# Kernel optimization log

Hardware: AMD Instinct MI355X
Metric: run time of the kernel (lower is better)

The kernel has to match this reference:

```python
import jax, jax.numpy as jnp
import numpy as np

P, N, M, B = 5, 30000, 50000, 256
T, C, L, ED, H, EMB, TD, NL = 13, 16, 3, 4, 128, 64, 5, 3
SRC = jnp.repeat(jnp.arange(P), P)  # edge type i = src*P + dst
DST = jnp.tile(jnp.arange(P), P)


def _affine(x, W, b):
    # x: [P, n, i], W: [P, i, o], b: [P, o]
    return jnp.einsum('pni,pio->pno', x, W) + b[:, None, :]


def _lrelu(x, s=0.01):
    return jnp.where(x >= 0, x, s * x)


def _gat(h, W, a_s, a_d, We, a_e, b, edge_index, edge_attr):
    # h: [P, N, H]; per-edge-type GATConv (heads=1, no self loops) then hetero 'max' aggregation
    hs, hd = h[SRC], h[DST]                       # [25, N, H]
    xl = jnp.einsum('enh,ehf->enf', hs, W)        # transformed source features
    xr = jnp.einsum('enh,ehf->enf', hd, W)
    als = jnp.einsum('enf,ef->en', xl, a_s)
    ald = jnp.einsum('enf,ef->en', xr, a_d)

    def per_type(xl_e, als_e, ald_e, ea, We_e, ae_e, ei):
        src, dst = ei[0], ei[1]
        alpha = als_e[src] + ald_e[dst] + (ea @ We_e) @ ae_e
        alpha = jnp.where(alpha >= 0, alpha, 0.2 * alpha)  # GAT negative_slope=0.2
        amax = jax.ops.segment_max(alpha, dst, num_segments=N)
        ex = jnp.exp(alpha - amax[dst])
        den = jax.ops.segment_sum(ex, dst, num_segments=N)
        w = ex / (den[dst] + 1e-16)
        return jax.ops.segment_sum(w[:, None] * xl_e[src], dst, num_segments=N)

    out = jax.vmap(per_type)(xl, als, ald, edge_attr, We, a_e, edge_index)
    out = out + b[:, None, :]
    return out.reshape(P, P, N, H).max(axis=0)  # HeteroConv aggr='max' over source types


def setup_inputs():
    key = jax.random.key(0)
    ks = iter(jax.random.split(key, 64))
    def nrm(shape, s=1.0):
        return jax.random.normal(next(ks), shape, dtype=jnp.float32) * s
    w = 0.05
    inp = {
        'x': nrm((P, N, T)),
        'cond_x': nrm((P, N, C + L)),
        'edge_attr': nrm((P * P, M, ED)),
        'timesteps': jax.random.uniform(next(ks), (B,), dtype=jnp.float32),
        'te1_W': nrm((1, TD), w), 'te1_b': nrm((TD,), w),
        'te2_W': nrm((TD, TD), w), 'te2_b': nrm((TD,), w),
        'emb_W': nrm((P, T + L, EMB), w), 'emb_b': nrm((P, EMB), w),
        'cemb_W': nrm((P, C, EMB), w), 'cemb_b': nrm((P, EMB), w),
        'pa_W': nrm((P, 2 * EMB, 2 * EMB), w), 'pa_b': nrm((P, 2 * EMB), w),
        'pc_W': nrm((P, 2 * EMB, EMB), w), 'pc_b': nrm((P, EMB), w),
        'sl0_W': nrm((P, EMB + TD, H), w), 'sl0_b': nrm((P, H), w),
        'sl12_W': nrm((2, P, H + TD, H), w), 'sl12_b': nrm((2, P, H), w),
        'slout_W': nrm((P, H + TD, T), w), 'slout_b': nrm((P, T), w),
        'gat_W': nrm((NL, P * P, H, H), w), 'gat_as': nrm((NL, P * P, H), w),
        'gat_ad': nrm((NL, P * P, H), w), 'gat_We': nrm((NL, P * P, ED, H), w),
        'gat_ae': nrm((NL, P * P, H), w), 'gat_b': nrm((NL, P * P, H), w),
        'xc_W': nrm((NL, P, H, H // 2), w), 'xc_b': nrm((NL, P, H // 2), w),
        'cc_W': nrm((NL, P, H, H // 2), w), 'cc_b': nrm((NL, P, H // 2), w),
        'ca_W': nrm((NL, P, H, H), w), 'ca_b': nrm((NL, P, H), w),
        'batch_idx': jax.random.randint(next(ks), (P, N), 0, B),
        'edge_index': jax.random.randint(next(ks), (P * P, 2, M), 0, N),
    }
    return inp


def reference(x, cond_x, edge_attr, timesteps, te1_W, te1_b, te2_W, te2_b,
              emb_W, emb_b, cemb_W, cemb_b, pa_W, pa_b, pc_W, pc_b,
              sl0_W, sl0_b, sl12_W, sl12_b, slout_W, slout_b,
              gat_W, gat_as, gat_ad, gat_We, gat_ae, gat_b,
              xc_W, xc_b, cc_W, cc_b, ca_W, ca_b, batch_idx, edge_index):
    # time embedding: Linear(1,TD) -> SiLU -> Linear(TD,TD)
    temb = jax.nn.silu(timesteps[:, None] @ te1_W + te1_b) @ te2_W + te2_b  # [B, TD]
    cond, latent = cond_x[..., :C], cond_x[..., C:]
    h = _affine(jnp.concatenate([x, latent], -1), emb_W, emb_b)            # [P,N,EMB]
    ce = _affine(cond, cemb_W, cemb_b)
    h = jnp.concatenate([h, ce], -1)                                       # [P,N,2EMB]
    h = jax.nn.sigmoid(_affine(h, pa_W, pa_b)) * h                         # attention pooling
    h = _affine(h, pc_W, pc_b)                                             # [P,N,EMB]
    nt = temb[batch_idx]                                                   # [P,N,TD]
    h = jnp.concatenate([h, nt], -1)
    for l in range(NL):
        if l > 0:
            h = jnp.concatenate([h, nt], -1)
        Wl, bl = (sl0_W, sl0_b) if l == 0 else (sl12_W[l - 1], sl12_b[l - 1])
        h = _lrelu(_affine(h, Wl, bl))                                     # [P,N,H]
        comm = _lrelu(_gat(h, gat_W[l], gat_as[l], gat_ad[l], gat_We[l], gat_ae[l], gat_b[l], edge_index, edge_attr))
        h = jnp.concatenate([_affine(h, xc_W[l], xc_b[l]), _affine(comm, cc_W[l], cc_b[l])], -1)
        h = h + jax.nn.sigmoid(_affine(h, ca_W[l], ca_b[l])) * h
    h = jnp.concatenate([h, nt], -1)
    return _affine(h, slout_W, slout_b)                                    # [P,N,T]
```

## Files before the change

### kernel.cpp

```cpp
#include <hip/hip_runtime.h>
#include <cstdio>

using bf8 = __attribute__((ext_vector_type(8))) short;
using f4v = __attribute__((ext_vector_type(4))) float;
typedef unsigned short u16;
typedef unsigned int u32;

#define DEV __device__ __forceinline__

DEV float bf2f(u16 u){ return __uint_as_float(((u32)u) << 16); }
DEV u16 f2bf(float f){ u32 u = __float_as_uint(f); return (u16)((u + 0x7fffu + ((u >> 16) & 1u)) >> 16); }
DEV float sigm(float v){ return 1.f / (1.f + __expf(-v)); }

constexpr int P5 = 5, NN = 30000, MM = 50000, NE = 25, BB = 256;
constexpr int KC = 96;
constexpr int RS = KC * 2 + 16;
constexpr int RSA = 272;

__global__ void temb_k(const float* ts, const float* w1, const float* b1,
                       const float* w2, const float* b2, float* temb){
  int i = blockIdx.x * blockDim.x + threadIdx.x;
  if (i >= BB) return;
  float t = ts[i]; float z[5];
#pragma unroll
  for (int j = 0; j < 5; ++j){ float u = t * w1[j] + b1[j]; z[j] = u * sigm(u); }
#pragma unroll
  for (int j2 = 0; j2 < 5; ++j2){
    float s = b2[j2];
#pragma unroll
    for (int j = 0; j < 5; ++j) s += z[j] * w2[j * 5 + j2];
    temb[i * 5 + j2] = s;
  }
}

__global__ void wtransE_k(const float* __restrict__ W, u16* __restrict__ Wt,
                          int Kreal, int Kpad, int Nreal, int Nalloc, int total){
  int idx = blockIdx.x * blockDim.x + threadIdx.x;
  if (idx >= total) return;
  int k = idx % Kpad;
  int t2 = idx / Kpad;
  int f = t2 % Nalloc;
  int b = t2 / Nalloc;
  float v = (k < Kreal && f < Nreal) ? W[((size_t)b * Kreal + k) * Nreal + f] : 0.f;
  Wt[idx] = f2bf(v);
}

__global__ void embw_k(const float* emb_W, const float* emb_b, const float* cemb_W, const float* cemb_b,
                       u16* Wc, float* bc){
  int b = blockIdx.x, f = threadIdx.x;
  for (int k = 0; k < 32; ++k){
    float v = 0.f;
    if (f < 64){ if (k < 16) v = emb_W[((size_t)b * 16 + k) * 64 + f]; }
    else       { if (k >= 16) v = cemb_W[((size_t)b * 16 + (k - 16)) * 64 + (f - 64)]; }
    Wc[((size_t)b * 128 + f) * 32 + k] = f2bf(v);
  }
  bc[b * 128 + f] = (f < 64) ? emb_b[b * 64 + f] : cemb_b[b * 64 + (f - 64)];
}

__global__ void gwtT_k(const float* __restrict__ gW, u16* __restrict__ gWt){
  int idx = blockIdx.x * blockDim.x + threadIdx.x;
  if (idx >= 75 * 128 * 128) return;
  int h = idx & 127, f = (idx >> 7) & 127, le = idx >> 14;
  gWt[idx] = f2bf(gW[(size_t)le * 16384 + h * 128 + f]);
}

__global__ void gatred_k(const float* gW, const float* gas, const float* gad,
                         const float* gWe, const float* gae,
                         float* wswd, float* eaw){
  int le = blockIdx.x; int h = threadIdx.x;
  const float* W = gW + (size_t)le * 16384;
  const float* as_ = gas + le * 128;
  const float* ad_ = gad + le * 128;
  float wsv = 0.f, wdv = 0.f;
  for (int f = 0; f < 128; ++f){
    float w = W[h * 128 + f];
    wsv += w * as_[f]; wdv += w * ad_[f];
  }
  wswd[le * 256 + h] = wsv;
  wswd[le * 256 + 128 + h] = wdv;
  if (h < 4){
    const float* We = gWe + (size_t)le * 512;
    const float* ae = gae + le * 128;
    float s = 0.f;
    for (int f = 0; f < 128; ++f) s += We[h * 128 + f] * ae[f];
    eaw[le * 4 + h] = s;
  }
}

__global__ void abuild_k(const float* x, const float* cx, u16* A0){
  int idx = blockIdx.x * blockDim.x + threadIdx.x;
  if (idx >= P5 * NN) return;
  const float* xr = x + (size_t)idx * 13;
  const float* cr = cx + (size_t)idx * 19;
  u16* a0 = A0 + (size_t)idx * 32;
#pragma unroll
  for (int i = 0; i < 13; ++i) a0[i] = f2bf(xr[i]);
#pragma unroll
  for (int i = 0; i < 3; ++i) a0[13 + i] = f2bf(cr[16 + i]);
#pragma unroll
  for (int i = 0; i < 16; ++i) a0[16 + i] = f2bf(cr[i]);
}

__global__ void ntfill_k(u16* buf, int pitch, int co, const int* bidx, const float* temb){
  int idx = blockIdx.x * blockDim.x + threadIdx.x;
  if (idx >= P5 * NN) return;
  int b = bidx[idx];
  u16* r = buf + (size_t)idx * pitch;
#pragma unroll
  for (int j = 0; j < 5; ++j) r[co + j] = f2bf(temb[b * 5 + j]);
  for (int j = co + 5; j < pitch; ++j) r[j] = 0;
}

__global__ void csr_count_k(const int* EI, int* cnt){
  int idx = blockIdx.x * blockDim.x + threadIdx.x;
  if (idx >= NE * MM) return;
  int e = idx / MM, m = idx % MM;
  int dst = EI[(size_t)e * 2 * MM + MM + m];
  atomicAdd(&cnt[e * NN + dst], 1);
}

__global__ __launch_bounds__(1024) void csr_scan_k(const int* cnt, int* off){
  int e = blockIdx.x, tid = threadIdx.x;
  int lane = tid & 63, wv = tid >> 6;
  __shared__ int wsum[16];
  int running = 0;
  for (int c = 0; c < 30; ++c){
    int idx = c * 1024 + tid;
    int v = (idx < NN) ? cnt[e * NN + idx] : 0;
    int s = v;
#pragma unroll
    for (int o = 1; o < 64; o <<= 1){
      int t = __shfl_up(s, o, 64);
      if (lane >= o) s += t;
    }
    if (lane == 63) wsum[wv] = s;
    __syncthreads();
    if (wv == 0 && lane < 16){
      int t = wsum[lane];
#pragma unroll
      for (int o = 1; o < 16; o <<= 1){
        int u = __shfl_up(t, o, 64);
        if (lane >= o) t += u;
      }
      wsum[lane] = t;
    }
    __syncthreads();
    int base = running + ((wv > 0) ? wsum[wv - 1] : 0);
    if (idx < NN) off[(size_t)e * (NN + 1) + idx] = base + s - v;
    running += wsum[15];
    __syncthreads();
  }
  if (tid == 0) off[(size_t)e * (NN + 1) + NN] = running;
}

__global__ void csr_fill_k(const int* EI, const int* off, int* cnt, int* mpos){
  int idx = blockIdx.x * blockDim.x + threadIdx.x;
  if (idx >= NE * MM) return;
  int e = idx / MM, m = idx % MM;
  int dst = EI[(size_t)e * 2 * MM + MM + m];
  int pos = off[(size_t)e * (NN + 1) + dst] + atomicAdd(&cnt[e * NN + dst], 1);
  mpos[idx] = pos;
}

__global__ __launch_bounds__(256) void dots2_k(const u16* __restrict__ hS, const float* __restrict__ wswd_l,
                                               float* __restrict__ als, float* __restrict__ ald){
  __shared__ u32 hl[64][65];
  __shared__ float wsl[10][129];
  int p = blockIdx.y;
  int n0 = blockIdx.x * 64;
  int tid = threadIdx.x;
  for (int i = tid; i < 10 * 128; i += 256){
    int col = i >> 7, k = i & 127;
    int e = (col < 5) ? (p * 5 + col) : ((col - 5) * 5 + p);
    wsl[col][k] = wswd_l[e * 256 + ((col < 5) ? 0 : 128) + k];
  }
  for (int i = tid; i < 64 * 64; i += 256){
    int r = i >> 6, kp = i & 63;
    int n = n0 + r;
    hl[r][kp] = (n < NN) ? ((const u32*)hS)[((size_t)p * NN + n) * 64 + kp] : 0u;
  }
  __syncthreads();
  int col = tid & 15, rbase = tid >> 4;
  if (col < 10){
#pragma unroll
    for (int pass = 0; pass < 4; ++pass){
      int r = rbase + pass * 16;
      int n = n0 + r;
      if (n >= NN) continue;
      float s = 0.f;
#pragma unroll
      for (int kp = 0; kp < 64; ++kp){
        u32 pr = hl[r][kp];
        s += bf2f((u16)(pr & 0xffffu)) * wsl[col][2 * kp]
           + bf2f((u16)(pr >> 16)) * wsl[col][2 * kp + 1];
      }
      if (col < 5) als[(size_t)(p * 5 + col) * NN + n] = s;
      else         ald[(size_t)((col - 5) * 5 + p) * NN + n] = s;
    }
  }
}

__global__ __launch_bounds__(256) void alpha_k(const int* EI, const float* ea, const float* als,
                                               const float* ald, const float* eaw_l,
                                               float* alpha, u32* amax){
  int idx = blockIdx.x * blockDim.x + threadIdx.x;
  if (idx >= NE * MM) return;
  int e = idx / MM, m = idx % MM;
  int src = EI[(size_t)e * 2 * MM + m];
  int dst = EI[(size_t)e * 2 * MM + MM + m];
  const float* a4 = ea + ((size_t)e * MM + m) * 4;
  const float* ew = eaw_l + e * 4;
  float a = als[(size_t)e * NN + src] + ald[(size_t)e * NN + dst]
          + a4[0] * ew[0] + a4[1] * ew[1] + a4[2] * ew[2] + a4[3] * ew[3];
  a = (a >= 0.f) ? a : 0.2f * a;
  alpha[(size_t)e * MM + m] = a;
  u32 ua = __float_as_uint(a);
  u32 enc = (ua & 0x80000000u) ? ~ua : (ua | 0x80000000u);
  atomicMax(&amax[(size_t)e * NN + dst], enc);
}

__global__ __launch_bounds__(256) void exprec_k(const int* EI, const float* alpha, const u32* amax,
                                                const int* mpos, uint2* prec){
  int idx = blockIdx.x * blockDim.x + threadIdx.x;
  if (idx >= NE * MM) return;
  int e = idx / MM, m = idx - e * MM;
  int src = EI[(size_t)e * 2 * MM + m];
  int dst = EI[(size_t)e * 2 * MM + MM + m];
  u32 enc = amax[(size_t)e * NN + dst];
  float am = (enc & 0x80000000u) ? __uint_as_float(enc & 0x7fffffffu) : __uint_as_float(~enc);
  float ex = __expf(alpha[idx] - am);
  uint2 pr; pr.x = (u32)src; pr.y = __float_as_uint(ex);
  prec[(size_t)e * MM + mpos[idx]] = pr;
}

__global__ __launch_bounds__(256) void agg3_k(const u16* __restrict__ hS, const uint2* __restrict__ prec,
                                              const int* __restrict__ off, u16* __restrict__ agghB,
                                              int pd0, int npd){
  int l = threadIdx.x & 63, w = threadIdx.x >> 6;
  int n0 = blockIdx.x * 8 + w;
  int n1 = n0 + 4;
  int y = blockIdx.y;
  int ps = y / npd, e = ps * 5 + pd0 + (y - ps * npd);
  const uint2* pe = prec + (size_t)e * MM;
  const int* offe = off + (size_t)e * (NN + 1);
  const u32* hb = (const u32*)hS + (size_t)ps * NN * 64 + l;
  int ro0 = 0, ln0 = 0, ro1 = 0, ln1 = 0;
  if (n0 < NN){ ro0 = offe[n0]; ln0 = offe[n0 + 1] - ro0; }
  if (n1 < NN){ ro1 = offe[n1]; ln1 = offe[n1 + 1] - ro1; }
  float den0 = 0.f, a00 = 0.f, a01 = 0.f;
  float den1 = 0.f, a10 = 0.f, a11 = 0.f;
  int mx = (ln0 > ln1) ? ln0 : ln1;
  for (int t = 0; t < mx; ++t){
    if (t < ln0){
      uint2 pr = pe[ro0 + t];
      float ex = __uint_as_float(pr.y);
      u32 hv = hb[(size_t)pr.x * 64];
      den0 += ex; a00 += ex * bf2f((u16)(hv & 0xffffu)); a01 += ex * bf2f((u16)(hv >> 16));
    }
    if (t < ln1){
      uint2 pr = pe[ro1 + t];
      float ex = __uint_as_float(pr.y);
      u32 hv = hb[(size_t)pr.x * 64];
      den1 += ex; a10 += ex * bf2f((u16)(hv & 0xffffu)); a11 += ex * bf2f((u16)(hv >> 16));
    }
  }
  if (n0 < NN){
    float inv = 1.f / (den0 + 1e-16f);
    ((u32*)agghB)[((size_t)y * NN + n0) * 64 + l] = (u32)f2bf(a00 * inv) | ((u32)f2bf(a01 * inv) << 16);
  }
  if (n1 < NN){
    float inv = 1.f / (den1 + 1e-16f);
    ((u32*)agghB)[((size_t)y * NN + n1) * 64 + l] = (u32)f2bf(a10 * inv) | ((u32)f2bf(a11 * inv) << 16);
  }
}

template<int NF, int MI, int NJ, int EPI, bool ALRELU>
__global__ __launch_bounds__(256) void tgemm_k(const u16* __restrict__ A, const u16* __restrict__ Wt,
                                               const float* __restrict__ bias, void* __restrict__ out,
                                               const u16* __restrict__ X,
                                               int Kpad, int opitch, int ocol, int xpitch){
  constexpr int Nalloc = NF * 16;
  constexpr int WR = 128 / (MI * 16);
  constexpr int WC = 4 / WR;
  static_assert(WR * WC == 4 && NJ * WC * 16 == Nalloc, "wave tiling");
  extern __shared__ __align__(16) char smem[];
  float* Cs = (float*)smem;
  const int tid = threadIdx.x;
  const int l = tid & 63, w = tid >> 6;
  const int bz = blockIdx.z;
  const int r0 = blockIdx.x * 128;
  const int wr = w / WC, wc = w % WC;
  const size_t Ab = (size_t)bz * NN;

  f4v acc[MI][NJ];
#pragma unroll
  for (int i = 0; i < MI; ++i)
#pragma unroll
    for (int j = 0; j < NJ; ++j) acc[i][j] = f4v{0.f, 0.f, 0.f, 0.f};

  for (int kb = 0; kb < Kpad; kb += KC){
    int kc = Kpad - kb; if (kc > KC) kc = KC;
    int nseg = kc >> 3;
    for (int s = tid; s < 128 * nseg; s += 256){
      int r = s / nseg, c = s - r * nseg;
      int grow = r0 + r; if (grow > NN - 1) grow = NN - 1;
      uint4 v = *(const uint4*)(A + (Ab + grow) * Kpad + kb + c * 8);
      if (ALRELU){
        u32 pr[4] = {v.x, v.y, v.z, v.w};
#pragma unroll
        for (int q = 0; q < 4; ++q){
          float lo = bf2f((u16)(pr[q] & 0xffffu)), hi = bf2f((u16)(pr[q] >> 16));
          lo = lo >= 0.f ? lo : 0.01f * lo; hi = hi >= 0.f ? hi : 0.01f * hi;
          pr[q] = (u32)f2bf(lo) | ((u32)f2bf(hi) << 16);
        }
        v.x = pr[0]; v.y = pr[1]; v.z = pr[2]; v.w = pr[3];
      }
      *(uint4*)(smem + r * RS + c * 16) = v;
    }
    for (int s = tid; s < Nalloc * nseg; s += 256){
      int r = s / nseg, c = s - r * nseg;
      uint4 v = *(const uint4*)(Wt + ((size_t)bz * Nalloc + r) * Kpad + kb + c * 8);
      *(uint4*)(smem + 128 * RS + r * RS + c * 16) = v;
    }
    __syncthreads();
    int KI = kc >> 5;
    for (int k0 = 0; k0 < KI; ++k0){
      bf8 af[MI], bfr[NJ];
#pragma unroll
      for (int i = 0; i < MI; ++i){
        int row = wr * (MI * 16) + i * 16 + (l & 15);
        af[i] = *(const bf8*)(smem + row * RS + k0 * 64 + (l >> 4) * 16);
      }
#pragma unroll
      for (int j = 0; j < NJ; ++j){
        int col = wc * (NJ * 16) + j * 16 + (l & 15);
        bfr[j] = *(const bf8*)(smem + 128 * RS + col * RS + k0 * 64 + (l >> 4) * 16);
      }
#pragma unroll
      for (int i = 0; i < MI; ++i)
#pragma unroll
        for (int j = 0; j < NJ; ++j)
          acc[i][j] = __builtin_amdgcn_mfma_f32_16x16x32_bf16(af[i], bfr[j], acc[i][j], 0, 0, 0);
    }
    __syncthreads();
  }

  if (EPI == 4){
    int col = l & 15;
    if (col < 13){
#pragma unroll
      for (int i = 0; i < MI; ++i){
        float bv = bias[bz * 13 + col];
#pragma unroll
        for (int r = 0; r < 4; ++r){
          int grow = r0 + wr * (MI * 16) + i * 16 + (l >> 4) * 4 + r;
          if (grow < NN)
            ((float*)out)[((size_t)bz * NN + grow) * 13 + col] = acc[i][0][r] + bv;
        }
      }
    }
    return;
  }

#pragma unroll
  for (int i = 0; i < MI; ++i)
#pragma unroll
    for (int j = 0; j < NJ; ++j){
      int tcol = wc * (NJ * 16) + j * 16 + (l & 15);
      float bv = bias[bz * Nalloc + tcol];
#pragma unroll
      for (int r = 0; r < 4; ++r){
        int trow = wr * (MI * 16) + i * 16 + (l >> 4) * 4 + r;
        float v = acc[i][j][r] + bv;
        if (EPI == 2) v = v >= 0.f ? v : 0.01f * v;
        Cs[trow * Nalloc + tcol] = v;
      }
    }
  __syncthreads();
  constexpr int nsc = Nalloc / 4;
  u16* o16 = (u16*)out;
  for (int s = tid; s < 128 * nsc; s += 256){
    int r = s / nsc, c = s - r * nsc;
    int grow = r0 + r; if (grow >= NN) continue;
    float4 cv = *(const float4*)(Cs + r * Nalloc + c * 4);
    float v0 = cv.x, v1 = cv.y, v2 = cv.z, v3 = cv.w;
    if (EPI == 1 || EPI == 3){
      uint2 xv = *(const uint2*)(X + ((size_t)bz * NN + grow) * xpitch + c * 4);
      float x0 = bf2f((u16)(xv.x & 0xffffu)), x1 = bf2f((u16)(xv.x >> 16));
      float x2 = bf2f((u16)(xv.y & 0xffffu)), x3 = bf2f((u16)(xv.y >> 16));
      if (EPI == 1){ v0 = x0 * sigm(v0); v1 = x1 * sigm(v1); v2 = x2 * sigm(v2); v3 = x3 * sigm(v3); }
      else { v0 = x0 * (1.f + sigm(v0)); v1 = x1 * (1.f + sigm(v1)); v2 = x2 * (1.f + sigm(v2)); v3 = x3 * (1.f + sigm(v3)); }
    }
    uint2 ov;
    ov.x = (u32)f2bf(v0) | ((u32)f2bf(v1) << 16);
    ov.y = (u32)f2bf(v2) | ((u32)f2bf(v3) << 16);
    *(uint2*)(o16 + ((size_t)bz * NN + grow) * opitch + ocol + c * 4) = ov;
  }
}

__global__ __launch_bounds__(256) void tgatmm_k(const u16* __restrict__ agghB, const u16* __restrict__ gWt_l,
                                                const float* __restrict__ gb_l, u16* __restrict__ comm,
                                                int pd){
  extern __shared__ __align__(16) char smem[];
  char* As = smem;
  char* Bs = smem + 128 * RSA;
  float* Cs = (float*)smem;
  const int tid = threadIdx.x, l = tid & 63, w = tid >> 6;
  const int r0 = blockIdx.x * 128;
  const int wr = w >> 1, wc = w & 1;
  f4v vmax[4][4];
#pragma unroll 1
  for (int ps = 0; ps < 5; ++ps){
    int e = ps * 5 + pd;
    const u16* aggs = agghB + (size_t)ps * NN * 128;
    const u16* wb = gWt_l + (size_t)e * 16384;
    for (int s = tid; s < 128 * 16; s += 256){
      int r = s >> 4, c = s & 15;
      int grow = r0 + r; if (grow > NN - 1) grow = NN - 1;
      *(uint4*)(As + r * RSA + c * 16) = *(const uint4*)(aggs + (size_t)grow * 128 + c * 8);
      *(uint4*)(Bs + r * RSA + c * 16) = *(const uint4*)(wb + r * 128 + c * 8);
    }
    __syncthreads();
    f4v acc[4][4];
#pragma unroll
    for (int i = 0; i < 4; ++i)
#pragma unroll
      for (int j = 0; j < 4; ++j) acc[i][j] = f4v{0.f, 0.f, 0.f, 0.f};
#pragma unroll
    for (int k0 = 0; k0 < 4; ++k0){
      bf8 af[4], bfr[4];
#pragma unroll
      for (int i = 0; i < 4; ++i)
        af[i] = *(const bf8*)(As + (wr * 64 + i * 16 + (l & 15)) * RSA + k0 * 64 + (l >> 4) * 16);
#pragma unroll
      for (int j = 0; j < 4; ++j)
        bfr[j] = *(const bf8*)(Bs + (wc * 64 + j * 16 + (l & 15)) * RSA + k0 * 64 + (l >> 4) * 16);
#pragma unroll
      for (int i = 0; i < 4; ++i)
#pragma unroll
        for (int j = 0; j < 4; ++j)
          acc[i][j] = __builtin_amdgcn_mfma_f32_16x16x32_bf16(af[i], bfr[j], acc[i][j], 0, 0, 0);
    }
    const float* be = gb_l + e * 128;
#pragma unroll
    for (int i = 0; i < 4; ++i)
#pragma unroll
      for (int j = 0; j < 4; ++j){
        int tcol = wc * 64 + j * 16 + (l & 15);
        float bv = be[tcol];
#pragma unroll
        for (int r = 0; r < 4; ++r){
          float cvv = acc[i][j][r] + bv;
          vmax[i][j][r] = (ps == 0) ? cvv : fmaxf(vmax[i][j][r], cvv);
        }
      }
    __syncthreads();
  }
#pragma unroll
  for (int i = 0; i < 4; ++i)
#pragma unroll
    for (int j = 0; j < 4; ++j){
      int tcol = wc * 64 + j * 16 + (l & 15);
#pragma unroll
      for (int r = 0; r < 4; ++r){
        int trow = wr * 64 + i * 16 + (l >> 4) * 4 + r;
        Cs[trow * 128 + tcol] = vmax[i][j][r];
      }
    }
  __syncthreads();
  for (int s = tid; s < 128 * 32; s += 256){
    int r = s >> 5, c = s & 31;
    int grow = r0 + r; if (grow >= NN) continue;
    float4 cv = *(const float4*)(Cs + r * 128 + c * 4);
    uint2 ov;
    ov.x = (u32)f2bf(cv.x) | ((u32)f2bf(cv.y) << 16);
    ov.y = (u32)f2bf(cv.z) | ((u32)f2bf(cv.w) << 16);
    *(uint2*)(comm + ((size_t)pd * NN + grow) * 128 + c * 4) = ov;
  }
}

constexpr size_t ALN(size_t x){ return (x + 255) & ~(size_t)255; }
constexpr size_t SZ_A0   = ALN((size_t)P5 * NN * 32 * 2);
constexpr size_t SZ_H0   = ALN((size_t)P5 * NN * 96 * 2);
constexpr size_t SZ_H128 = ALN((size_t)P5 * NN * 128 * 2);
constexpr size_t SZ_HL   = ALN((size_t)P5 * NN * 160 * 2);
constexpr size_t O_A0 = 0;
constexpr size_t O_H0 = O_A0 + SZ_A0;
constexpr size_t O_AGG = 0;
constexpr size_t O_HCAT = O_H0 + SZ_H0;
constexpr size_t O_HG = O_HCAT + SZ_H128;
constexpr size_t O_HS = O_HG + SZ_H128;
constexpr size_t O_HL = O_HS + SZ_H128;
constexpr size_t O_TEMB = O_HL + SZ_HL;
constexpr size_t O_WSWD = O_TEMB + ALN(256 * 5 * 4);
constexpr size_t O_EAW  = O_WSWD + ALN(75 * 256 * 4);
constexpr size_t O_CNT  = O_EAW + ALN(75 * 4 * 4);
constexpr size_t O_OFFS = O_CNT + ALN((size_t)NE * NN * 4);
constexpr size_t O_MPOS = O_OFFS + ALN((size_t)NE * (NN + 1) * 4);
constexpr size_t O_ALS  = O_MPOS + ALN((size_t)NE * MM * 4);
constexpr size_t O_ALD  = O_ALS + ALN((size_t)NE * NN * 4);
constexpr size_t O_ALPHA= O_ALD + ALN((size_t)NE * NN * 4);
constexpr size_t O_AMAX = O_ALPHA + ALN((size_t)NE * MM * 4);
constexpr size_t O_GWT  = O_AMAX + ALN((size_t)NE * NN * 4);
constexpr size_t O_WCMB = O_GWT + ALN((size_t)75 * 16384 * 2);
constexpr size_t O_BCMB = O_WCMB + ALN((size_t)5 * 128 * 32 * 2);
constexpr size_t O_WPA  = O_BCMB + ALN((size_t)5 * 128 * 4);
constexpr size_t O_WPC  = O_WPA + ALN((size_t)5 * 128 * 128 * 2);
constexpr size_t O_WSL0 = O_WPC + ALN((size_t)5 * 64 * 128 * 2);
constexpr size_t O_WSL12= O_WSL0 + ALN((size_t)5 * 128 * 96 * 2);
constexpr size_t O_WSLO = O_WSL12 + ALN((size_t)10 * 128 * 160 * 2);
constexpr size_t O_WXC  = O_WSLO + ALN((size_t)5 * 16 * 160 * 2);
constexpr size_t O_WCC  = O_WXC + ALN((size_t)15 * 64 * 128 * 2);
constexpr size_t O_WCA  = O_WCC + ALN((size_t)15 * 64 * 128 * 2);
constexpr size_t O_PREC = O_WCA + ALN((size_t)15 * 128 * 128 * 2);
constexpr size_t WS_NEED= O_PREC + ALN((size_t)NE * MM * 8);

extern "C" void kernel_launch(void* const* d_in, const int* in_sizes, int n_in,
                              void* d_out, int out_size, void* d_ws, size_t ws_size,
                              hipStream_t stream){
  if (ws_size < WS_NEED){
    fprintf(stderr, "kernel_launch: ws too small: need %zu have %zu\n", WS_NEED, ws_size);
    return;
  }
  const float* x        = (const float*)d_in[0];
  const float* cond_x   = (const float*)d_in[1];
  const float* edge_attr= (const float*)d_in[2];
  const float* timesteps= (const float*)d_in[3];
  const float* te1_W = (const float*)d_in[4];
  const float* te1_b = (const float*)d_in[5];
  const float* te2_W = (const float*)d_in[6];
  const float* te2_b = (const float*)d_in[7];
  const float* emb_W = (const float*)d_in[8];
  const float* emb_b = (const float*)d_in[9];
  const float* cemb_W= (const float*)d_in[10];
  const float* cemb_b= (const float*)d_in[11];
  const float* pa_W  = (const float*)d_in[12];
  const float* pa_b  = (const float*)d_in[13];
  const float* pc_W  = (const float*)d_in[14];
  const float* pc_b  = (const float*)d_in[15];
  const float* sl0_W = (const float*)d_in[16];
  const float* sl0_b = (const float*)d_in[17];
  const float* sl12_W= (const float*)d_in[18];
  const float* sl12_b= (const float*)d_in[19];
  const float* slout_W=(const float*)d_in[20];
  const float* slout_b=(const float*)d_in[21];
  const float* gat_W = (const float*)d_in[22];
  const float* gat_as= (const float*)d_in[23];
  const float* gat_ad= (const float*)d_in[24];
  const float* gat_We= (const float*)d_in[25];
  const float* gat_ae= (const float*)d_in[26];
  const float* gat_b = (const float*)d_in[27];
  const float* xc_W  = (const float*)d_in[28];
  const float* xc_b  = (const float*)d_in[29];
  const float* cc_W  = (const float*)d_in[30];
  const float* cc_b  = (const float*)d_in[31];
  const float* ca_W  = (const float*)d_in[32];
  const float* ca_b  = (const float*)d_in[33];
  const int* batch_idx = (const int*)d_in[34];
  const int* edge_index= (const int*)d_in[35];

  char* ws = (char*)d_ws;
  u16* A0    = (u16*)(ws + O_A0);
  u16* h0buf = (u16*)(ws + O_H0);
  u16* agghB = (u16*)(ws + O_AGG);
  u16* hcat  = (u16*)(ws + O_HCAT);
  u16* hg    = (u16*)(ws + O_HG);
  u16* h2    = (u16*)(ws + O_HG);
  u16* hS    = (u16*)(ws + O_HS);
  u16* hL    = (u16*)(ws + O_HL);
  u16* comm  = (u16*)(ws + O_HL);
  float* tembp = (float*)(ws + O_TEMB);
  float* wswdp = (float*)(ws + O_WSWD);
  float* eawp  = (float*)(ws + O_EAW);
  int* cnt  = (int*)(ws + O_CNT);
  int* offs = (int*)(ws + O_OFFS);
  int* mposp= (int*)(ws + O_MPOS);
  float* alsp = (float*)(ws + O_ALS);
  float* aldp = (float*)(ws + O_ALD);
  float* alphap = (float*)(ws + O_ALPHA);
  u32* amaxp = (u32*)(ws + O_AMAX);
  u16* gwt   = (u16*)(ws + O_GWT);
  u16* wcmb  = (u16*)(ws + O_WCMB);
  float* bcmb= (float*)(ws + O_BCMB);
  u16* wpa   = (u16*)(ws + O_WPA);
  u16* wpc   = (u16*)(ws + O_WPC);
  u16* wsl0  = (u16*)(ws + O_WSL0);
  u16* wsl12 = (u16*)(ws + O_WSL12);
  u16* wslo  = (u16*)(ws + O_WSLO);
  u16* wxc   = (u16*)(ws + O_WXC);
  u16* wcc   = (u16*)(ws + O_WCC);
  u16* wca   = (u16*)(ws + O_WCA);
  uint2* precp = (uint2*)(ws + O_PREC);

  const dim3 B256(256);
  const dim3 TG(235, 1, 5);
  const int GPN = (P5 * NN + 255) / 256;
  const int GEM = (NE * MM + 255) / 256;
  constexpr int LDS_N128 = 65536;
  constexpr int LDS_N64  = 39936;
  constexpr int LDS_SLO  = 29952;
  constexpr int LDS_TGAT = 128 * RSA * 2;

  temb_k<<<1, B256, 0, stream>>>(timesteps, te1_W, te1_b, te2_W, te2_b, tembp);
  embw_k<<<5, 128, 0, stream>>>(emb_W, emb_b, cemb_W, cemb_b, wcmb, bcmb);
  {
    auto WT = [&](const float* W, u16* Wt, int Kr, int Kp, int Nr, int Na, int B){
      int total = B * Na * Kp;
      wtransE_k<<<(total + 255) / 256, B256, 0, stream>>>(W, Wt, Kr, Kp, Nr, Na, total);
    };
    WT(pa_W, wpa, 128, 128, 128, 128, 5);
    WT(pc_W, wpc, 128, 128, 64, 64, 5);
    WT(sl0_W, wsl0, 69, 96, 128, 128, 5);
    WT(sl12_W, wsl12, 133, 160, 128, 128, 10);
    WT(slout_W, wslo, 133, 160, 13, 16, 5);
    WT(xc_W, wxc, 128, 128, 64, 64, 15);
    WT(cc_W, wcc, 128, 128, 64, 64, 15);
    WT(ca_W, wca, 128, 128, 128, 128, 15);
  }
  gwtT_k<<<(75 * 128 * 128 + 255) / 256, B256, 0, stream>>>(gat_W, gwt);
  gatred_k<<<75, 128, 0, stream>>>(gat_W, gat_as, gat_ad, gat_We, gat_ae, wswdp, eawp);

  hipMemsetAsync(cnt, 0, (size_t)NE * NN * 4, stream);
  csr_count_k<<<GEM, B256, 0, stream>>>(edge_index, cnt);
  csr_scan_k<<<25, 1024, 0, stream>>>(cnt, offs);
  hipMemsetAsync(cnt, 0, (size_t)NE * NN * 4, stream);
  csr_fill_k<<<GEM, B256, 0, stream>>>(edge_index, offs, cnt, mposp);

  abuild_k<<<GPN, B256, 0, stream>>>(x, cond_x, A0);
  tgemm_k<8, 4, 4, 0, false><<<TG, B256, LDS_N128, stream>>>(A0, wcmb, bcmb, hcat, nullptr, 32, 128, 0, 0);
  tgemm_k<8, 4, 4, 1, false><<<TG, B256, LDS_N128, stream>>>(hcat, wpa, pa_b, hg, hcat, 128, 128, 0, 128);
  tgemm_k<4, 2, 4, 0, false><<<TG, B256, LDS_N64, stream>>>(hg, wpc, pc_b, h0buf, nullptr, 128, 96, 0, 0);
  ntfill_k<<<GPN, B256, 0, stream>>>(h0buf, 96, 64, batch_idx, tembp);

  for (int l = 0; l < 3; ++l){
    if (l == 0)
      tgemm_k<8, 4, 4, 2, false><<<TG, B256, LDS_N128, stream>>>(h0buf, wsl0, sl0_b, hS, nullptr, 96, 128, 0, 0);
    else
      tgemm_k<8, 4, 4, 2, false><<<TG, B256, LDS_N128, stream>>>(hL, wsl12 + (size_t)(l - 1) * 5 * 128 * 160,
                                                                 sl12_b + (size_t)(l - 1) * 5 * 128, hS, nullptr,
                                                                 160, 128, 0, 0);
    const float* wswd_l = wswdp + (size_t)l * 25 * 256;
    const float* eaw_l = eawp + (size_t)l * 25 * 4;
    const u16* gwt_l = gwt + (size_t)l * 25 * 16384;
    const float* gb_l = gat_b + (size_t)l * 25 * 128;
    dots2_k<<<dim3(469, 5), B256, 0, stream>>>(hS, wswd_l, alsp, aldp);
    hipMemsetAsync(amaxp, 0, (size_t)NE * NN * 4, stream);
    alpha_k<<<GEM, B256, 0, stream>>>(edge_index, edge_attr, alsp, aldp, eaw_l, alphap, amaxp);
    exprec_k<<<GEM, B256, 0, stream>>>(edge_index, alphap, amaxp, mposp, precp);
    for (int pd = 0; pd < 5; ++pd){
      agg3_k<<<dim3(3750, 5), B256, 0, stream>>>(hS, precp, offs, agghB, pd, 1);
      tgatmm_k<<<dim3(235), B256, LDS_TGAT, stream>>>(agghB, gwt_l, gb_l, comm, pd);
    }
    tgemm_k<4, 2, 4, 0, false><<<TG, B256, LDS_N64, stream>>>(hS, wxc + (size_t)l * 5 * 64 * 128,
                                                              xc_b + (size_t)l * 5 * 64, h2, nullptr,
                                                              128, 128, 0, 0);
    tgemm_k<4, 2, 4, 0, true><<<TG, B256, LDS_N64, stream>>>(comm, wcc + (size_t)l * 5 * 64 * 128,
                                                             cc_b + (size_t)l * 5 * 64, h2, nullptr,
                                                             128, 128, 64, 0);
    tgemm_k<8, 4, 4, 3, false><<<TG, B256, LDS_N128, stream>>>(h2, wca + (size_t)l * 5 * 128 * 128,
                                                               ca_b + (size_t)l * 5 * 128, hL, h2,
                                                               128, 160, 0, 128);
    ntfill_k<<<GPN, B256, 0, stream>>>(hL, 160, 128, batch_idx, tembp);
  }

  tgemm_k<1, 2, 1, 4, false><<<TG, B256, LDS_SLO, stream>>>(hL, wslo, slout_b, d_out, nullptr, 160, 13, 0, 0);
}
```

Measured before the change: 2.061 ms.

## Compute GAT softmax per destination via CSR, removing atomics and alpha buffer

```diff
diff --git a/kernel.cpp b/kernel.cpp
--- a/kernel.cpp
+++ b/kernel.cpp
@@ -153,13 +153,27 @@
   if (tid == 0) off[(size_t)e * (NN + 1) + NN] = running;
 }
 
-__global__ void csr_fill_k(const int* EI, const int* off, int* cnt, int* mpos){
+__global__ void csr_fill_k(const int* EI, const int* off, int* cnt, int* mpos, int* srcC){
   int idx = blockIdx.x * blockDim.x + threadIdx.x;
   if (idx >= NE * MM) return;
   int e = idx / MM, m = idx % MM;
   int dst = EI[(size_t)e * 2 * MM + MM + m];
   int pos = off[(size_t)e * (NN + 1) + dst] + atomicAdd(&cnt[e * NN + dst], 1);
   mpos[idx] = pos;
+  srcC[(size_t)e * MM + pos] = EI[(size_t)e * 2 * MM + m];
+}
+
+__global__ void eadot_k(const float* __restrict__ ea, const float* __restrict__ eaw,
+                        const int* __restrict__ mpos, float* __restrict__ eadot){
+  int idx = blockIdx.x * blockDim.x + threadIdx.x;
+  if (idx >= 3 * NE * MM) return;
+  int l = idx / (NE * MM);
+  int rem = idx - l * NE * MM;
+  int e = rem / MM, m = rem - e * MM;
+  const float* a4 = ea + ((size_t)e * MM + m) * 4;
+  const float* ew = eaw + (size_t)(l * NE + e) * 4;
+  float d = a4[0] * ew[0] + a4[1] * ew[1] + a4[2] * ew[2] + a4[3] * ew[3];
+  eadot[(size_t)l * NE * MM + (size_t)e * MM + mpos[rem]] = d;
 }
 
 __global__ __launch_bounds__(256) void dots2_k(const u16* __restrict__ hS, const float* __restrict__ wswd_l,
@@ -200,37 +214,31 @@
   }
 }
 
-__global__ __launch_bounds__(256) void alpha_k(const int* EI, const float* ea, const float* als,
-                                               const float* ald, const float* eaw_l,
-                                               float* alpha, u32* amax){
-  int idx = blockIdx.x * blockDim.x + threadIdx.x;
-  if (idx >= NE * MM) return;
-  int e = idx / MM, m = idx % MM;
-  int src = EI[(size_t)e * 2 * MM + m];
-  int dst = EI[(size_t)e * 2 * MM + MM + m];
-  const float* a4 = ea + ((size_t)e * MM + m) * 4;
-  const float* ew = eaw_l + e * 4;
-  float a = als[(size_t)e * NN + src] + ald[(size_t)e * NN + dst]
-          + a4[0] * ew[0] + a4[1] * ew[1] + a4[2] * ew[2] + a4[3] * ew[3];
-  a = (a >= 0.f) ? a : 0.2f * a;
-  alpha[(size_t)e * MM + m] = a;
-  u32 ua = __float_as_uint(a);
-  u32 enc = (ua & 0x80000000u) ? ~ua : (ua | 0x80000000u);
-  atomicMax(&amax[(size_t)e * NN + dst], enc);
-}
-
-__global__ __launch_bounds__(256) void exprec_k(const int* EI, const float* alpha, const u32* amax,
-                                                const int* mpos, uint2* prec){
-  int idx = blockIdx.x * blockDim.x + threadIdx.x;
-  if (idx >= NE * MM) return;
-  int e = idx / MM, m = idx - e * MM;
-  int src = EI[(size_t)e * 2 * MM + m];
-  int dst = EI[(size_t)e * 2 * MM + MM + m];
-  u32 enc = amax[(size_t)e * NN + dst];
-  float am = (enc & 0x80000000u) ? __uint_as_float(enc & 0x7fffffffu) : __uint_as_float(~enc);
-  float ex = __expf(alpha[idx] - am);
-  uint2 pr; pr.x = (u32)src; pr.y = __float_as_uint(ex);
-  prec[(size_t)e * MM + mpos[idx]] = pr;
+__global__ __launch_bounds__(256) void aexp_k(const float* __restrict__ als, const float* __restrict__ ald,
+                                              const float* __restrict__ eadot_l, const int* __restrict__ srcC,
+                                              const int* __restrict__ off, uint2* __restrict__ prec){
+  int idx = blockIdx.x * blockDim.x + threadIdx.x;
+  if (idx >= NE * NN) return;
+  int e = idx / NN;
+  int ro = off[(size_t)e + idx], re = off[(size_t)e + idx + 1];
+  if (ro >= re) return;
+  float av = ald[idx];
+  const int* sc = srcC + (size_t)e * MM;
+  const float* ed = eadot_l + (size_t)e * MM;
+  const float* ale = als + (size_t)e * NN;
+  float mx = -3.0e38f;
+  for (int j = ro; j < re; ++j){
+    float a = ale[sc[j]] + av + ed[j];
+    a = (a >= 0.f) ? a : 0.2f * a;
+    mx = fmaxf(mx, a);
+  }
+  for (int j = ro; j < re; ++j){
+    int src = sc[j];
+    float a = ale[src] + av + ed[j];
+    a = (a >= 0.f) ? a : 0.2f * a;
+    uint2 pr; pr.x = (u32)src; pr.y = __float_as_uint(__expf(a - mx));
+    prec[(size_t)e * MM + j] = pr;
+  }
 }
 
 __global__ __launch_bounds__(256) void agg3_k(const u16* __restrict__ hS, const uint2* __restrict__ prec,
@@ -499,9 +507,9 @@
 constexpr size_t O_MPOS = O_OFFS + ALN((size_t)NE * (NN + 1) * 4);
 constexpr size_t O_ALS  = O_MPOS + ALN((size_t)NE * MM * 4);
 constexpr size_t O_ALD  = O_ALS + ALN((size_t)NE * NN * 4);
-constexpr size_t O_ALPHA= O_ALD + ALN((size_t)NE * NN * 4);
-constexpr size_t O_AMAX = O_ALPHA + ALN((size_t)NE * MM * 4);
-constexpr size_t O_GWT  = O_AMAX + ALN((size_t)NE * NN * 4);
+constexpr size_t O_SRCC = O_ALD + ALN((size_t)NE * NN * 4);
+constexpr size_t O_EADOT= O_SRCC + ALN((size_t)NE * MM * 4);
+constexpr size_t O_GWT  = O_EADOT + ALN((size_t)3 * NE * MM * 4);
 constexpr size_t O_WCMB = O_GWT + ALN((size_t)75 * 16384 * 2);
 constexpr size_t O_BCMB = O_WCMB + ALN((size_t)5 * 128 * 32 * 2);
 constexpr size_t O_WPA  = O_BCMB + ALN((size_t)5 * 128 * 4);
@@ -577,8 +585,8 @@
   int* mposp= (int*)(ws + O_MPOS);
   float* alsp = (float*)(ws + O_ALS);
   float* aldp = (float*)(ws + O_ALD);
-  float* alphap = (float*)(ws + O_ALPHA);
-  u32* amaxp = (u32*)(ws + O_AMAX);
+  int* srcCp = (int*)(ws + O_SRCC);
+  float* eadotp = (float*)(ws + O_EADOT);
   u16* gwt   = (u16*)(ws + O_GWT);
   u16* wcmb  = (u16*)(ws + O_WCMB);
   float* bcmb= (float*)(ws + O_BCMB);
@@ -596,6 +604,7 @@
   const dim3 TG(235, 1, 5);
   const int GPN = (P5 * NN + 255) / 256;
   const int GEM = (NE * MM + 255) / 256;
+  const int GEN = (NE * NN + 255) / 256;
   constexpr int LDS_N128 = 65536;
   constexpr int LDS_N64  = 39936;
   constexpr int LDS_SLO  = 29952;
@@ -624,7 +633,8 @@
   csr_count_k<<<GEM, B256, 0, stream>>>(edge_index, cnt);
   csr_scan_k<<<25, 1024, 0, stream>>>(cnt, offs);
   hipMemsetAsync(cnt, 0, (size_t)NE * NN * 4, stream);
-  csr_fill_k<<<GEM, B256, 0, stream>>>(edge_index, offs, cnt, mposp);
+  csr_fill_k<<<GEM, B256, 0, stream>>>(edge_index, offs, cnt, mposp, srcCp);
+  eadot_k<<<(3 * NE * MM + 255) / 256, B256, 0, stream>>>(edge_attr, eawp, mposp, eadotp);
 
   abuild_k<<<GPN, B256, 0, stream>>>(x, cond_x, A0);
   tgemm_k<8, 4, 4, 0, false><<<TG, B256, LDS_N128, stream>>>(A0, wcmb, bcmb, hcat, nullptr, 32, 128, 0, 0);
@@ -640,13 +650,10 @@
                                                                  sl12_b + (size_t)(l - 1) * 5 * 128, hS, nullptr,
                                                                  160, 128, 0, 0);
     const float* wswd_l = wswdp + (size_t)l * 25 * 256;
-    const float* eaw_l = eawp + (size_t)l * 25 * 4;
     const u16* gwt_l = gwt + (size_t)l * 25 * 16384;
     const float* gb_l = gat_b + (size_t)l * 25 * 128;
     dots2_k<<<dim3(469, 5), B256, 0, stream>>>(hS, wswd_l, alsp, aldp);
-    hipMemsetAsync(amaxp, 0, (size_t)NE * NN * 4, stream);
-    alpha_k<<<GEM, B256, 0, stream>>>(edge_index, edge_attr, alsp, aldp, eaw_l, alphap, amaxp);
-    exprec_k<<<GEM, B256, 0, stream>>>(edge_index, alphap, amaxp, mposp, precp);
+    aexp_k<<<GEN, B256, 0, stream>>>(alsp, aldp, eadotp + (size_t)l * NE * MM, srcCp, offs, precp);
     for (int pd = 0; pd < 5; ++pd){
       agg3_k<<<dim3(3750, 5), B256, 0, stream>>>(hS, precp, offs, agghB, pd, 1);
       tgatmm_k<<<dim3(235), B256, LDS_TGAT, stream>>>(agghB, gwt_l, gb_l, comm, pd);
```

Result: faster. 1.956 ms (-5.1%).
